# Optimization experiments

Hardware: AMD Instinct MI355X
Metric: run time of the kernel (lower is better)

## Reference

```python
import jax, jax.numpy as jnp
import numpy as np

D_MODEL = 1024
NUM_HEADS = 16
D_K = D_MODEL // NUM_HEADS


def setup_inputs() -> dict:
    key = jax.random.key(0)
    ks = jax.random.split(key, 11)
    B, S = 2, 2048
    scale = 1.0 / np.sqrt(D_MODEL)
    return {
        "Q": jax.random.normal(ks[0], (B, S, D_MODEL), jnp.float32),
        "K": jax.random.normal(ks[1], (B, S, D_MODEL), jnp.float32),
        "V": jax.random.normal(ks[2], (B, S, D_MODEL), jnp.float32),
        "Wq": jax.random.normal(ks[3], (D_MODEL, D_MODEL), jnp.float32) * scale,
        "bq": jnp.zeros((D_MODEL,), jnp.float32),
        "Wk": jax.random.normal(ks[4], (D_MODEL, D_MODEL), jnp.float32) * scale,
        "bk": jnp.zeros((D_MODEL,), jnp.float32),
        "Wv": jax.random.normal(ks[5], (D_MODEL, D_MODEL), jnp.float32) * scale,
        "bv": jnp.zeros((D_MODEL,), jnp.float32),
        "Wo": jax.random.normal(ks[6], (D_MODEL, D_MODEL), jnp.float32) * scale,
        "bo": jnp.zeros((D_MODEL,), jnp.float32),
    }


def reference(Q, K, V, Wq, bq, Wk, bk, Wv, bv, Wo, bo):
    B, S, _ = Q.shape
    # linear projections (torch Linear: x @ W.T + b)
    q = Q @ Wq.T + bq
    k = K @ Wk.T + bk
    v = V @ Wv.T + bv
    # split heads: [B, S, H, d_k] -> [B, H, S, d_k]
    q = q.reshape(B, S, NUM_HEADS, D_K).transpose(0, 2, 1, 3)
    k = k.reshape(B, S, NUM_HEADS, D_K).transpose(0, 2, 1, 3)
    v = v.reshape(B, S, NUM_HEADS, D_K).transpose(0, 2, 1, 3)
    # scaled dot-product attention, full [B, H, S, S] scores as in original
    scores = jnp.einsum("bhqd,bhkd->bhqk", q, k) / jnp.sqrt(jnp.float32(D_K))
    probs = jax.nn.softmax(scores, axis=-1)
    attn = jnp.einsum("bhqk,bhkd->bhqd", probs, v)
    # merge heads and output projection
    attn = attn.transpose(0, 2, 1, 3).reshape(B, S, D_MODEL)
    return attn @ Wo.T + bo
```

## Files before the change

### kernel.cpp

```cpp
#include <hip/hip_runtime.h>
#include <cstdint>
#include <cstddef>

#define D_MODEL 1024
#define NHEADS 16
#define DK 64
#define BATCH 2
#define SEQ 2048
#define MROWS 4096

using f32x4 = __attribute__((ext_vector_type(4))) float;
using f32x16 = __attribute__((ext_vector_type(16))) float;
using u16x8 = __attribute__((ext_vector_type(8))) unsigned short;
using u32x4 = __attribute__((ext_vector_type(4))) unsigned int;
using bf16x8 = __attribute__((ext_vector_type(8))) __bf16;

static __device__ __forceinline__ f32x4 mfma16(u16x8 a, u16x8 b, f32x4 c) {
    return __builtin_amdgcn_mfma_f32_16x16x32_bf16(
        __builtin_bit_cast(bf16x8, a), __builtin_bit_cast(bf16x8, b), c, 0, 0, 0);
}
static __device__ __forceinline__ f32x16 mfma32(u16x8 a, u16x8 b, f32x16 c) {
    return __builtin_amdgcn_mfma_f32_32x32x16_bf16(
        __builtin_bit_cast(bf16x8, a), __builtin_bit_cast(bf16x8, b), c, 0, 0, 0);
}

static __device__ __forceinline__ unsigned short f2b(float f) {
    unsigned int u = __float_as_uint(f);
    u += 0x7fffu + ((u >> 16) & 1u);
    return (unsigned short)(u >> 16);
}
static __device__ __forceinline__ unsigned int cvt_pk(float lo, float hi) {
    unsigned int r;
    asm("v_cvt_pk_bf16_f32 %0, %1, %2" : "=v"(r) : "v"(lo), "v"(hi));
    return r;
}
static __device__ __forceinline__ void plswap(unsigned int& a, unsigned int& b) {
    asm("v_permlane32_swap_b32 %0, %1" : "+v"(a), "+v"(b));
}
static __device__ __forceinline__ float fexp2(float x) {
#if __has_builtin(__builtin_amdgcn_exp2f)
    return __builtin_amdgcn_exp2f(x);
#else
    float r;
    asm("v_exp_f32 %0, %1" : "=v"(r) : "v"(x));
    return r;
#endif
}
static __device__ __forceinline__ void gll16(const void* g, void* l) {
    __builtin_amdgcn_global_load_lds(
        (const __attribute__((address_space(1))) void*)g,
        (__attribute__((address_space(3))) void*)l, 16, 0, 0);
}
#define SBAR() __builtin_amdgcn_s_barrier()
#define SCHED0() __builtin_amdgcn_sched_barrier(0)
#define WAITV(n) asm volatile("s_waitcnt vmcnt(" #n ")" ::: "memory")

__global__ __launch_bounds__(256) void cvt_flat_kernel(
    const float* __restrict__ w0, const float* __restrict__ w1,
    const float* __restrict__ w2, const float* __restrict__ w3,
    const float* __restrict__ a0, const float* __restrict__ a1,
    const float* __restrict__ a2,
    unsigned short* __restrict__ outW, unsigned short* __restrict__ outA,
    float scale0) {
    const int c = ((int)blockIdx.x * 256 + (int)threadIdx.x) * 4;
    const float* src;
    ushort4* dst;
    float scale = 1.0f;
    if (c < 1048576) {
        const float* ws[4] = {w0, w1, w2, w3};
        int m = c >> 18;
        int off = c & 262143;
        src = ws[m] + (size_t)off * 4;
        dst = reinterpret_cast<ushort4*>(outW) + ((size_t)m << 18) + off;
        if (m == 0) scale = scale0;
    } else {
        int ai = c - 1048576;
        const float* as[3] = {a0, a1, a2};
        int m = ai >> 20;
        int off = ai & 1048575;
        src = as[m] + (size_t)off * 4;
        dst = reinterpret_cast<ushort4*>(outA) + ((size_t)m << 20) + off;
    }
    float4 v0 = reinterpret_cast<const float4*>(src)[0];
    float4 v1 = reinterpret_cast<const float4*>(src)[1];
    float4 v2 = reinterpret_cast<const float4*>(src)[2];
    float4 v3 = reinterpret_cast<const float4*>(src)[3];
    ushort4 o0 = {f2b(v0.x * scale), f2b(v0.y * scale), f2b(v0.z * scale), f2b(v0.w * scale)};
    ushort4 o1 = {f2b(v1.x * scale), f2b(v1.y * scale), f2b(v1.z * scale), f2b(v1.w * scale)};
    ushort4 o2 = {f2b(v2.x * scale), f2b(v2.y * scale), f2b(v2.z * scale), f2b(v2.w * scale)};
    ushort4 o3 = {f2b(v3.x * scale), f2b(v3.y * scale), f2b(v3.z * scale), f2b(v3.w * scale)};
    dst[0] = o0;
    dst[1] = o1;
    dst[2] = o2;
    dst[3] = o3;
}


__global__ __launch_bounds__(256, 4) void gemm_qkv_kernel(
    const unsigned short* __restrict__ Abf,
    const unsigned short* __restrict__ W,
    unsigned short* __restrict__ qo, unsigned short* __restrict__ ko,
    unsigned short* __restrict__ vto,
    const float* __restrict__ b0, const float* __restrict__ b1, const float* __restrict__ b2,
    float qsc) {
    __shared__ __align__(16) char Ab[2][8192];
    __shared__ __align__(16) char Wb[2][8192];

    const int tid = threadIdx.x;
    const int lane = tid & 63;
    const int wid = tid >> 6;
    const int wr = wid >> 1, wc = wid & 1;
    const int g = (lane >> 4) & 3, l16 = lane & 15;

    const int logical = ((int)blockIdx.x & 7) * 96 + ((int)blockIdx.x >> 3);
    const int m = logical >> 8;
    const int rem = logical & 255;
    const int y = rem >> 3, xc = rem & 7;
    const int row0 = y * 128;
    const int arow0 = m * MROWS + row0;
    const int wrow0 = m * 1024 + xc * 128;

    const int sline = tid >> 3;
    const int sgl = (tid & 7) ^ (sline & 7);
    const int srow = sline * 2 + (sgl >> 2);
    const int skcol = (sgl & 3) * 8;

    auto stage = [&](int k0, int buf) {
        const char* a0 = (const char*)Abf + (size_t)(arow0 + srow) * 2048 + (size_t)(k0 + skcol) * 2;
        gll16(a0, Ab[buf] + wid * 1024);
        gll16(a0 + (size_t)64 * 2048, Ab[buf] + 4096 + wid * 1024);
        const char* w0 = (const char*)W + (size_t)(wrow0 + srow) * 2048 + (size_t)(k0 + skcol) * 2;
        gll16(w0, Wb[buf] + wid * 1024);
        gll16(w0 + (size_t)64 * 2048, Wb[buf] + 4096 + wid * 1024);
    };

    const int rswz = ((((l16 & 1) << 2) + g) ^ ((l16 >> 1) & 7)) << 4;
    const int abase = (wr * 32 + (l16 >> 1)) * 128 + rswz;
    const int bbase = (wc * 32 + (l16 >> 1)) * 128 + rswz;

    f32x4 acc[4][4] = {};
    stage(0, 0);

    for (int t = 0; t < 32; ++t) {
        if (t < 31) stage((t + 1) * 32, (t & 1) ^ 1);
        if (t < 31) WAITV(4);
        else WAITV(0);
        SCHED0();
        SBAR();
        SCHED0();
        u16x8 af[4], bf[4];
#pragma unroll
        for (int mi = 0; mi < 4; ++mi)
            af[mi] = *reinterpret_cast<const u16x8*>(Ab[t & 1] + abase + mi * 1024);
#pragma unroll
        for (int ni = 0; ni < 4; ++ni)
            bf[ni] = *reinterpret_cast<const u16x8*>(Wb[t & 1] + bbase + ni * 1024);
        __builtin_amdgcn_s_setprio(1);
#pragma unroll
        for (int mi = 0; mi < 4; ++mi)
#pragma unroll
            for (int ni = 0; ni < 4; ++ni)
                acc[mi][ni] = mfma16(af[mi], bf[ni], acc[mi][ni]);
        __builtin_amdgcn_s_setprio(0);
        SBAR();
        SCHED0();
    }

    const float* bias = (m == 0) ? b0 : ((m == 1) ? b1 : b2);
    const float bsc = (m == 0) ? qsc : 1.0f;
#pragma unroll
    for (int mi = 0; mi < 4; ++mi) {
#pragma unroll
        for (int ni = 0; ni < 4; ++ni) {
            int r = row0 + wr * 64 + mi * 16 + g * 4;
            int cl = xc * 128 + wc * 64 + ni * 16 + l16;
            float bv = bsc * bias[cl];
            if (m < 2) {
                unsigned short* outp = m ? ko : qo;
#pragma unroll
                for (int j = 0; j < 4; ++j)
                    outp[(size_t)(r + j) * 1024 + cl] = f2b(acc[mi][ni][j] + bv);
            } else {
                ushort4 o;
                o.x = f2b(acc[mi][ni][0] + bv);
                o.y = f2b(acc[mi][ni][1] + bv);
                o.z = f2b(acc[mi][ni][2] + bv);
                o.w = f2b(acc[mi][ni][3] + bv);
                *reinterpret_cast<ushort4*>(vto + (size_t)cl * MROWS + r) = o;
            }
        }
    }
}

__global__ __launch_bounds__(256, 4) void gemm_out_kernel(
    const unsigned short* __restrict__ Abf,
    const unsigned short* __restrict__ W,
    float* __restrict__ fo,
    const float* __restrict__ bias) {
    __shared__ __align__(16) char Ab[2][8192];
    __shared__ __align__(16) char Wb[2][4096];

    const int tid = threadIdx.x;
    const int lane = tid & 63;
    const int wid = tid >> 6;
    const int wr = wid >> 1, wc = wid & 1;
    const int g = (lane >> 4) & 3, l16 = lane & 15;

    const int logical = ((int)blockIdx.x & 7) * 64 + ((int)blockIdx.x >> 3);
    const int y = logical >> 4, xc = logical & 15;
    const int row0 = y * 128;
    const int wrow0 = xc * 64;

    const int sline = tid >> 3;
    const int sgl = (tid & 7) ^ (sline & 7);
    const int srow = sline * 2 + (sgl >> 2);
    const int skcol = (sgl & 3) * 8;

    auto stage = [&](int k0, int buf) {
        const char* a0 = (const char*)Abf + (size_t)(row0 + srow) * 2048 + (size_t)(k0 + skcol) * 2;
        gll16(a0, Ab[buf] + wid * 1024);
        gll16(a0 + (size_t)64 * 2048, Ab[buf] + 4096 + wid * 1024);
        const char* w0 = (const char*)W + (size_t)(wrow0 + srow) * 2048 + (size_t)(k0 + skcol) * 2;
        gll16(w0, Wb[buf] + wid * 1024);
    };

    const int rswz = ((((l16 & 1) << 2) + g) ^ ((l16 >> 1) & 7)) << 4;
    const int abase = (wr * 32 + (l16 >> 1)) * 128 + rswz;
    const int bbase = (wc * 16 + (l16 >> 1)) * 128 + rswz;

    f32x4 acc[4][2] = {};
    stage(0, 0);

    for (int t = 0; t < 32; ++t) {
        if (t < 31) stage((t + 1) * 32, (t & 1) ^ 1);
        if (t < 31) WAITV(3);
        else WAITV(0);
        SCHED0();
        SBAR();
        SCHED0();
        u16x8 af[4], bf[2];
#pragma unroll
        for (int mi = 0; mi < 4; ++mi)
            af[mi] = *reinterpret_cast<const u16x8*>(Ab[t & 1] + abase + mi * 1024);
#pragma unroll
        for (int ni = 0; ni < 2; ++ni)
            bf[ni] = *reinterpret_cast<const u16x8*>(Wb[t & 1] + bbase + ni * 1024);
        __builtin_amdgcn_s_setprio(1);
#pragma unroll
        for (int mi = 0; mi < 4; ++mi)
#pragma unroll
            for (int ni = 0; ni < 2; ++ni)
                acc[mi][ni] = mfma16(af[mi], bf[ni], acc[mi][ni]);
        __builtin_amdgcn_s_setprio(0);
        SBAR();
        SCHED0();
    }

#pragma unroll
    for (int mi = 0; mi < 4; ++mi) {
#pragma unroll
        for (int ni = 0; ni < 2; ++ni) {
            int r = row0 + wr * 64 + mi * 16 + g * 4;
            int cl = xc * 64 + wc * 32 + ni * 16 + l16;
            float bv = bias[cl];
#pragma unroll
            for (int j = 0; j < 4; ++j)
                fo[(size_t)(r + j) * 1024 + cl] = acc[mi][ni][j] + bv;
        }
    }
}

__global__ __launch_bounds__(512, 2) void attn_kernel(
    const unsigned short* __restrict__ qp,
    const unsigned short* __restrict__ kp,
    const unsigned short* __restrict__ vT,
    unsigned short* __restrict__ ao) {
    __shared__ __align__(16) char lds[49152];

    const int tid = threadIdx.x;
    const int lane = tid & 63;
    const int wid = tid >> 6;
    const int wq = wid & 1, wk = wid >> 1;
    const int l31 = lane & 31, hi = lane >> 5;

    const int logical = ((int)blockIdx.x & 7) * 128 + ((int)blockIdx.x >> 3);
    const int qtile = logical & 31;
    const int bh = logical >> 5;
    const int b = bh >> 4, h = bh & 15;
    const int ch = h * DK;
    const int q0 = b * SEQ + qtile * 64;

    const int klp = (tid >> 4) & 15;
    const int kgl = (tid & 15) ^ klp;
    const int krow2 = klp * 2 + (kgl >> 3);
    const int koct = kgl & 7;
    const char* ksrc0 = (const char*)kp +
        ((size_t)(b * SEQ + (tid >> 8) * 512 + krow2)) * 2048 + ch * 2 + koct * 16;
    const int vd = tid >> 4;
    const int vglog = (tid & 15) ^ (vd & 15);
    const char* vsrc0 = (const char*)vT +
        ((size_t)(ch + vd)) * (MROWS * 2) +
        ((size_t)(b * SEQ + (vglog >> 2) * 512 + (vglog & 3) * 8)) * 2;

    const char* qr = (const char*)qp + (size_t)(q0 + wq * 32 + l31) * 2048 + ch * 2;
    u16x8 qf[4];
#pragma unroll
    for (int t = 0; t < 4; ++t)
        qf[t] = *reinterpret_cast<const u16x8*>(qr + t * 32 + hi * 16);

    char* kbuf = lds;
    char* vbuf = lds + 16384;

    auto stageK = [&](int kt2) {
        gll16(ksrc0 + (size_t)kt2 * 65536, kbuf + wid * 1024);
        gll16(ksrc0 + (size_t)kt2 * 65536 + (size_t)1024 * 2048, kbuf + 8192 + wid * 1024);
    };
    auto stageV = [&](int kt2, int buf) {
        char* base = vbuf + (buf << 14);
        gll16(vsrc0 + kt2 * 64, base + wid * 1024);
        gll16(vsrc0 + (size_t)32 * (MROWS * 2) + kt2 * 64, base + 8192 + wid * 1024);
    };

    f32x16 acco[2] = {};
    float l0 = 0.f, l1 = 0.f, l2 = 0.f, l3 = 0.f;

    stageV(0, 0);
    stageK(0);
    for (int kt = 0; kt < 16; ++kt) {
        if (kt < 15) {
            stageV(kt + 1, (kt + 1) & 1);
            WAITV(2);
        } else {
            WAITV(0);
        }
        SCHED0();
        SBAR();
        SCHED0();

        f32x16 s = {};
        __builtin_amdgcn_s_setprio(1);
#pragma unroll
        for (int t = 0; t < 4; ++t) {
            u16x8 kf = *reinterpret_cast<const u16x8*>(
                kbuf + (wk * 16 + (l31 >> 1)) * 256 +
                (((((l31 & 1) << 3) + 2 * t + hi) ^ ((l31 >> 1) & 15)) << 4));
            s = mfma32(kf, qf[t], s);
        }
        __builtin_amdgcn_s_setprio(0);
        SBAR();
        SCHED0();
        if (kt < 15) stageK(kt + 1);

        float p[16];
#pragma unroll
        for (int r = 0; r < 16; r += 4) {
            p[r] = fexp2(s[r]);
            p[r + 1] = fexp2(s[r + 1]);
            p[r + 2] = fexp2(s[r + 2]);
            p[r + 3] = fexp2(s[r + 3]);
            l0 += p[r];
            l1 += p[r + 1];
            l2 += p[r + 2];
            l3 += p[r + 3];
        }
        unsigned int pf0[4], pf1[4];
#pragma unroll
        for (int i = 0; i < 2; ++i) {
            unsigned int a = cvt_pk(p[2 * i], p[2 * i + 1]);
            unsigned int bb = cvt_pk(p[4 + 2 * i], p[5 + 2 * i]);
            plswap(a, bb);
            pf0[i] = a;
            pf0[i + 2] = bb;
            unsigned int a2 = cvt_pk(p[8 + 2 * i], p[9 + 2 * i]);
            unsigned int b2 = cvt_pk(p[12 + 2 * i], p[13 + 2 * i]);
            plswap(a2, b2);
            pf1[i] = a2;
            pf1[i + 2] = b2;
        }

        const char* Vb = vbuf + ((kt & 1) << 14);
        __builtin_amdgcn_s_setprio(1);
#pragma unroll
        for (int t = 0; t < 2; ++t) {
            u32x4 wv = t ? u32x4{pf1[0], pf1[1], pf1[2], pf1[3]}
                         : u32x4{pf0[0], pf0[1], pf0[2], pf0[3]};
            u16x8 pfr = __builtin_bit_cast(u16x8, wv);
#pragma unroll
            for (int dt = 0; dt < 2; ++dt) {
                u16x8 vf = *reinterpret_cast<const u16x8*>(
                    Vb + (dt * 32 + l31) * 256 + (((wk * 4 + 2 * t + hi) ^ (l31 & 15)) << 4));
                acco[dt] = mfma32(vf, pfr, acco[dt]);
            }
        }
        __builtin_amdgcn_s_setprio(0);
        SBAR();
        SCHED0();
    }

    float Lh = ((l0 + l1) + (l2 + l3));
    Lh += __shfl_xor(Lh, 32);

    float* cmb = reinterpret_cast<float*>(lds);
    if (wk >= 2) {
        float* slot = cmb + (size_t)((((wk - 2) * 2 + wq) * 64) + lane) * 34;
#pragma unroll
        for (int dt = 0; dt < 2; ++dt)
#pragma unroll
            for (int mm = 0; mm < 8; ++mm)
                *reinterpret_cast<float2*>(slot + dt * 16 + 2 * mm) =
                    float2{acco[dt][2 * mm], acco[dt][2 * mm + 1]};
        slot[32] = Lh;
    }
    __syncthreads();
    if (wk < 2) {
        const float* s2 = cmb + (size_t)(((wk * 2 + wq) * 64) + lane) * 34;
#pragma unroll
        for (int dt = 0; dt < 2; ++dt)
#pragma unroll
            for (int mm = 0; mm < 8; ++mm) {
                float2 t2 = *reinterpret_cast<const float2*>(s2 + dt * 16 + 2 * mm);
                acco[dt][2 * mm] += t2.x;
                acco[dt][2 * mm + 1] += t2.y;
            }
        Lh += s2[32];
    }
    __syncthreads();
    if (wk == 1) {
        float* slot = cmb + (size_t)((wq * 64) + lane) * 34;
#pragma unroll
        for (int dt = 0; dt < 2; ++dt)
#pragma unroll
            for (int mm = 0; mm < 8; ++mm)
                *reinterpret_cast<float2*>(slot + dt * 16 + 2 * mm) =
                    float2{acco[dt][2 * mm], acco[dt][2 * mm + 1]};
        slot[32] = Lh;
    }
    __syncthreads();
    if (wk == 0) {
        const float* s2 = cmb + (size_t)((wq * 64) + lane) * 34;
#pragma unroll
        for (int dt = 0; dt < 2; ++dt)
#pragma unroll
            for (int mm = 0; mm < 8; ++mm) {
                float2 t2 = *reinterpret_cast<const float2*>(s2 + dt * 16 + 2 * mm);
                acco[dt][2 * mm] += t2.x;
                acco[dt][2 * mm + 1] += t2.y;
            }
        Lh += s2[32];
    }
    __syncthreads();

    if (wk == 0) {
        float rl = 1.0f / Lh;
        const int r7 = l31 & 7;
        const int rr = lane >> 1, half = lane & 1;
        const int rb7 = rr & 7;
#pragma unroll
        for (int dt = 0; dt < 2; ++dt) {
            char* ot = lds + 36864 + (wid * 2 + dt) * 2304;
#pragma unroll
            for (int mm = 0; mm < 4; ++mm) {
                uint2 pko;
                pko.x = cvt_pk(acco[dt][4 * mm] * rl, acco[dt][4 * mm + 1] * rl);
                pko.y = cvt_pk(acco[dt][4 * mm + 2] * rl, acco[dt][4 * mm + 3] * rl);
                *reinterpret_cast<uint2*>(ot + l31 * 72 + (((2 * mm + hi) ^ r7) << 3)) = pko;
            }
            uint2 t0 = *reinterpret_cast<const uint2*>(ot + rr * 72 + (((half * 4 + 0) ^ rb7) << 3));
            uint2 t1 = *reinterpret_cast<const uint2*>(ot + rr * 72 + (((half * 4 + 1) ^ rb7) << 3));
            uint2 t2 = *reinterpret_cast<const uint2*>(ot + rr * 72 + (((half * 4 + 2) ^ rb7) << 3));
            uint2 t3 = *reinterpret_cast<const uint2*>(ot + rr * 72 + (((half * 4 + 3) ^ rb7) << 3));
            unsigned short* dst = ao + (size_t)(q0 + wq * 32 + rr) * 1024 + ch + dt * 32 + half * 16;
            uint4 o0 = {t0.x, t0.y, t1.x, t1.y};
            uint4 o1 = {t2.x, t2.y, t3.x, t3.y};
            *reinterpret_cast<uint4*>(dst) = o0;
            *reinterpret_cast<uint4*>(dst + 8) = o1;
        }
    }
}

extern "C" void kernel_launch(void* const* d_in, const int* in_sizes, int n_in,
                              void* d_out, int out_size, void* d_ws, size_t ws_size,
                              hipStream_t stream) {
    const float* Q = (const float*)d_in[0];
    const float* K = (const float*)d_in[1];
    const float* V = (const float*)d_in[2];
    const float* Wq = (const float*)d_in[3];
    const float* bq = (const float*)d_in[4];
    const float* Wk = (const float*)d_in[5];
    const float* bk = (const float*)d_in[6];
    const float* Wv = (const float*)d_in[7];
    const float* bv = (const float*)d_in[8];
    const float* Wo = (const float*)d_in[9];
    const float* bo = (const float*)d_in[10];

    unsigned short* ws = (unsigned short*)d_ws;
    const size_t SZ = (size_t)MROWS * D_MODEL;
    const size_t WSZ = (size_t)D_MODEL * D_MODEL;
    unsigned short* bufW = ws;
    unsigned short* abf = bufW + 4 * WSZ;
    unsigned short* qp = abf + 3 * SZ;
    unsigned short* kp = qp + SZ;
    unsigned short* vT = kp + SZ;
    unsigned short* ao = vT + SZ;

    const float qscale = 0.125f * 1.44269504088896f;

    dim3 blk(256);
    cvt_flat_kernel<<<dim3(4096), blk, 0, stream>>>(Wq, Wk, Wv, Wo, Q, K, V, bufW, abf, qscale);

    gemm_qkv_kernel<<<dim3(768), blk, 0, stream>>>(abf, bufW, qp, kp, vT, bq, bk, bv, qscale);

    attn_kernel<<<dim3(1024), dim3(512), 0, stream>>>(qp, kp, vT, ao);

    gemm_out_kernel<<<dim3(512), blk, 0, stream>>>(ao, bufW + 3 * WSZ, (float*)d_out, bo);
}
```

Before: 120.9 us.

## Stage V tiles through registers into single LDS buffer to shrink shared memory

Replaces the double-buffered direct global-to-LDS V staging with a register prefetch: each iteration loads the next V tile into registers, then writes it to a single LDS buffer after the end-of-iteration barrier. This cuts the attention kernel's LDS from 48KB to 34KB, probably so more workgroups can be resident per CU, and the output staging area is moved to the start of LDS to match. In exchange it adds VGPR pressure, extra LDS write instructions and lgkmcnt waits on the critical path between iterations.

After: 121.2 us. About the same (+0.2%).

```diff
diff --git a/kernel.cpp b/kernel.cpp
--- a/kernel.cpp
+++ b/kernel.cpp
@@ -54,6 +54,7 @@
 #define SBAR() __builtin_amdgcn_s_barrier()
 #define SCHED0() __builtin_amdgcn_sched_barrier(0)
 #define WAITV(n) asm volatile("s_waitcnt vmcnt(" #n ")" ::: "memory")
+#define WAITL0() asm volatile("s_waitcnt lgkmcnt(0)" ::: "memory")
 
 __global__ __launch_bounds__(256) void cvt_flat_kernel(
     const float* __restrict__ w0, const float* __restrict__ w1,
@@ -275,7 +276,7 @@
     const unsigned short* __restrict__ kp,
     const unsigned short* __restrict__ vT,
     unsigned short* __restrict__ ao) {
-    __shared__ __align__(16) char lds[49152];
+    __shared__ __align__(16) char lds[34816];
 
     const int tid = threadIdx.x;
     const int lane = tid & 63;
@@ -315,20 +316,32 @@
         gll16(ksrc0 + (size_t)kt2 * 65536, kbuf + wid * 1024);
         gll16(ksrc0 + (size_t)kt2 * 65536 + (size_t)1024 * 2048, kbuf + 8192 + wid * 1024);
     };
-    auto stageV = [&](int kt2, int buf) {
-        char* base = vbuf + (buf << 14);
-        gll16(vsrc0 + kt2 * 64, base + wid * 1024);
-        gll16(vsrc0 + (size_t)32 * (MROWS * 2) + kt2 * 64, base + 8192 + wid * 1024);
+
+    u16x8 vr0, vr1;
+    auto loadVregs = [&](int kt2) {
+        vr0 = *reinterpret_cast<const u16x8*>(vsrc0 + kt2 * 64);
+        vr1 = *reinterpret_cast<const u16x8*>(vsrc0 + (size_t)32 * (MROWS * 2) + kt2 * 64);
+    };
+    auto writeV = [&]() {
+        *reinterpret_cast<u16x8*>(vbuf + tid * 16) = vr0;
+        *reinterpret_cast<u16x8*>(vbuf + 8192 + tid * 16) = vr1;
     };
 
     f32x16 acco[2] = {};
     float l0 = 0.f, l1 = 0.f, l2 = 0.f, l3 = 0.f;
 
-    stageV(0, 0);
+    loadVregs(0);
     stageK(0);
+    WAITV(2);
+    SCHED0();
+    writeV();
+    WAITL0();
+    SCHED0();
+
     for (int kt = 0; kt < 16; ++kt) {
         if (kt < 15) {
-            stageV(kt + 1, (kt + 1) & 1);
+            loadVregs(kt + 1);
+            SCHED0();
             WAITV(2);
         } else {
             WAITV(0);
@@ -378,7 +391,6 @@
             pf1[i + 2] = b2;
         }
 
-        const char* Vb = vbuf + ((kt & 1) << 14);
         __builtin_amdgcn_s_setprio(1);
 #pragma unroll
         for (int t = 0; t < 2; ++t) {
@@ -388,13 +400,20 @@
 #pragma unroll
             for (int dt = 0; dt < 2; ++dt) {
                 u16x8 vf = *reinterpret_cast<const u16x8*>(
-                    Vb + (dt * 32 + l31) * 256 + (((wk * 4 + 2 * t + hi) ^ (l31 & 15)) << 4));
+                    vbuf + (dt * 32 + l31) * 256 + (((wk * 4 + 2 * t + hi) ^ (l31 & 15)) << 4));
                 acco[dt] = mfma32(vf, pfr, acco[dt]);
             }
         }
         __builtin_amdgcn_s_setprio(0);
         SBAR();
         SCHED0();
+        if (kt < 15) {
+            WAITV(2);
+            SCHED0();
+            writeV();
+            WAITL0();
+            SCHED0();
+        }
     }
 
     float Lh = ((l0 + l1) + (l2 + l3));
@@ -457,7 +476,7 @@
         const int rb7 = rr & 7;
 #pragma unroll
         for (int dt = 0; dt < 2; ++dt) {
-            char* ot = lds + 36864 + (wid * 2 + dt) * 2304;
+            char* ot = lds + (wid * 2 + dt) * 2304;
 #pragma unroll
             for (int mm = 0; mm < 4; ++mm) {
                 uint2 pko;
```
